# Kernel tuning notes

Hardware: AMD Instinct MI355X
Metric: run time of the kernel (lower is better)

Reference implementation:

```python
import jax, jax.numpy as jnp
import numpy as np

N_NODES = 15000
N_EDGES = 300000
N_RADIAL = 8
N_SPEC = 16
ZMAX = 64
CUTOFF = 5.0
LMAX = 2
NCHANNELS = 128


def bessel_basis(r, dim, rc):
    # b_n(r) = sqrt(2/rc) * sin(n*pi*r/rc) / r , n = 1..dim
    n = jnp.arange(1, dim + 1, dtype=r.dtype)
    return jnp.sqrt(2.0 / rc) * jnp.sin(n[None, :] * (jnp.pi / rc) * r[:, None]) / r[:, None]


def spherical_harmonics_l2(u):
    # Real solid harmonics of unit vectors up to l=2 (Racah/L2-style constants), 9 components
    x, y, z = u[:, 0], u[:, 1], u[:, 2]
    s3 = 3.0 ** 0.5
    s5 = 5.0 ** 0.5
    s15 = 15.0 ** 0.5
    one = jnp.ones_like(x)
    return jnp.stack([
        one,
        s3 * x, s3 * y, s3 * z,
        s15 * x * y, s15 * y * z,
        0.5 * s5 * (3.0 * z * z - 1.0),
        s15 * x * z, 0.5 * s15 * (x * x - y * y),
    ], axis=-1)  # [E, 9]


def setup_inputs() -> dict:
    key = jax.random.key(0)
    ks = jax.random.split(key, 8)
    vec = jax.random.normal(ks[0], (N_EDGES, 3), dtype=jnp.float32)
    distances = jnp.linalg.norm(vec, axis=-1) + 1e-3  # positive, consistent with vec
    switch = jax.random.uniform(ks[1], (N_EDGES,), dtype=jnp.float32)
    species_table = jax.random.normal(ks[2], (ZMAX, N_SPEC), dtype=jnp.float32)
    nbasis = N_RADIAL * N_SPEC
    W0 = jax.random.normal(ks[3], (nbasis, 2 * NCHANNELS), dtype=jnp.float32) / jnp.sqrt(nbasis)
    W1 = jax.random.normal(ks[4], (nbasis, 2 * NCHANNELS), dtype=jnp.float32) / jnp.sqrt(nbasis)
    W2 = jax.random.normal(ks[5], (nbasis, 2 * NCHANNELS), dtype=jnp.float32) / jnp.sqrt(nbasis)
    species = jax.random.randint(ks[6], (N_NODES,), 0, ZMAX)
    edge_src = jnp.sort(jax.random.randint(ks[7], (N_EDGES,), 0, N_NODES))
    edge_dst = jax.random.randint(jax.random.fold_in(key, 7), (N_EDGES,), 0, N_NODES)
    return {
        "distances": distances, "vec": vec, "switch": switch,
        "species_table": species_table, "W0": W0, "W1": W1, "W2": W2,
        "species": species, "edge_src": edge_src, "edge_dst": edge_dst,
    }


def reference(distances, vec, switch, species_table, W0, W1, W2, species, edge_src, edge_dst):
    n_nodes = species.shape[0]
    # radial basis * switch: [E, nr]
    rb = bessel_basis(distances, N_RADIAL, CUTOFF) * switch[:, None]
    senc = species_table[species]  # [N, ns]
    # edge-wise outer product radial x species -> [E, nr*ns]
    Dij = (rb[:, :, None] * senc[edge_dst, None, :]).reshape(rb.shape[0], -1)
    Y = spherical_harmonics_l2(vec / distances[:, None])  # [E, 9]
    # outer product with SH then scatter-sum to nodes: [N, 9, nbasis]
    rhoi = jax.ops.segment_sum(Dij[:, None, :] * Y[:, :, None], edge_src, num_segments=n_nodes)
    xis = [senc, rhoi[:, 0, :]]
    for l, W in enumerate((W0, W1, W2)):
        rhoil = rhoi[:, l * l:(l + 1) * (l + 1), :]  # [N, 2l+1, nbasis]
        xy = jnp.einsum('nmb,bc->nmc', rhoil, W)      # [N, 2l+1, 2*nchannels]
        xl, yl = jnp.split(xy, 2, axis=-1)
        xis.append((xl * yl).sum(axis=1) / (2 * l + 1) ** 0.5)
    return jnp.concatenate(xis, axis=-1)  # [N, ns + nbasis + 3*nchannels]
```

## Files before the change

### kernel.cpp

```cpp
#include <hip/hip_runtime.h>
#include <math.h>

#define N_NODES 15000
#define NPAD    15008
#define N_EDGES 300000
#define NCH     128
#define OUT_COLS 528
#define ES      300032
#define NCHUNK  (ES / 32)
#define YROWS   17
#define CHB     (YROWS * 32)

typedef _Float16 half8   __attribute__((ext_vector_type(8)));
typedef short    short8  __attribute__((ext_vector_type(8)));
typedef float    floatx4 __attribute__((ext_vector_type(4)));

#define WF_BYTES    (3 * 256 * 128 * 2)
#define RP_OFF      WF_BYTES
#define RP_BYTES    61440
#define SPE_OFF     (RP_OFF + RP_BYTES)
#define SPE_BYTES   ((size_t)ES * 2)
#define YF_OFF      (SPE_OFF + SPE_BYTES)
#define YF_BYTES    ((size_t)NCHUNK * CHB * 2 + 256)

#define PREP_EDGE_BLOCKS 1172
#define PREP_WF_BLOCKS   384
#define PREP_RP_BLOCKS   59
#define PREP_BLOCKS (PREP_EDGE_BLOCKS + PREP_WF_BLOCKS + PREP_RP_BLOCKS)

__device__ __forceinline__ size_t wf_pos(int l, int c, int k) {
    int h = c >> 7, cc = c & 127;
    int ct = cc >> 4, nI = cc & 15;
    int K = k >> 5, q = (k >> 3) & 3, j = k & 7;
    return ((size_t)((((l * 8 + ct) * 2 + h) * 4 + K) * 64 + q * 16 + nI)) * 8 + j;
}

__global__ __launch_bounds__(256) void prep_kernel(
    const float* __restrict__ dist, const float* __restrict__ vec,
    const float* __restrict__ sw,   const int* __restrict__ species,
    const int* __restrict__ edst,   const int* __restrict__ esrc,
    const float* __restrict__ W0, const float* __restrict__ W1,
    const float* __restrict__ W2,
    _Float16* __restrict__ Yf, short* __restrict__ spE,
    _Float16* __restrict__ WF,  int* __restrict__ row_ptr)
{
    const int b = blockIdx.x, tid = threadIdx.x;
    if (b < PREP_EDGE_BLOCKS) {
        int e = b * 256 + tid;
        if (e >= N_EDGES) return;

        const float bnorm = 0.6324555320336759f;
        const float s3  = 1.7320508075688772f;
        const float s5  = 2.2360679774997896f;
        const float s15 = 3.872983346207417f;
        const float cstep = 3.14159265358979323846f / 5.0f;

        float r    = dist[e];
        float invr = 1.0f / r;
        float g    = bnorm * invr * sw[e];
        float x = vec[3*e+0] * invr;
        float y = vec[3*e+1] * invr;
        float z = vec[3*e+2] * invr;

        spE[e] = (short)species[edst[e]];

        _Float16* yb = Yf + (size_t)(e >> 5) * CHB + (e & 31);
        yb[0 * 32] = (_Float16)1.0f;
        yb[1 * 32] = (_Float16)(s3 * x);
        yb[2 * 32] = (_Float16)(s3 * y);
        yb[3 * 32] = (_Float16)(s3 * z);
        yb[4 * 32] = (_Float16)(s15 * x * y);
        yb[5 * 32] = (_Float16)(s15 * y * z);
        yb[6 * 32] = (_Float16)(0.5f * s5 * (3.0f * z * z - 1.0f));
        yb[7 * 32] = (_Float16)(s15 * x * z);
        yb[8 * 32] = (_Float16)(0.5f * s15 * (x * x - y * y));
        #pragma unroll
        for (int n = 0; n < 8; ++n)
            yb[(9 + n) * 32] = (_Float16)(g * __sinf((float)(n + 1) * cstep * r));
    } else if (b < PREP_EDGE_BLOCKS + PREP_WF_BLOCKS) {
        int idx = (b - PREP_EDGE_BLOCKS) * 256 + tid;
        int l = idx >> 15;
        int c = (idx >> 7) & 255;
        int k = idx & 127;
        const float* W = (l == 0) ? W0 : ((l == 1) ? W1 : W2);
        WF[wf_pos(l, c, k)] = (_Float16)W[k * 256 + c];
    } else {
        int i = (b - PREP_EDGE_BLOCKS - PREP_WF_BLOCKS) * 256 + tid;
        if (i > NPAD) return;
        int lo = 0, hi = N_EDGES;
        while (lo < hi) { int mid = (lo + hi) >> 1; if (esrc[mid] < i) lo = mid + 1; else hi = mid; }
        row_ptr[i] = lo;
    }
}

__global__ __launch_bounds__(256) void main_kernel(
    const _Float16* __restrict__ Yf, const short* __restrict__ spE,
    const float* __restrict__ stab,  const int* __restrict__ row_ptr,
    const _Float16* __restrict__ WF, const int* __restrict__ species,
    float* __restrict__ out)
{
    __shared__ _Float16 stabL[64 * 16];
    __shared__ __align__(16) _Float16 srho[144 * 136];

    const int tid  = threadIdx.x;
    const int wave = tid >> 6;
    const int lane = tid & 63;
    const int q    = lane >> 4;
    const int nI   = lane & 15;
    const int node0 = blockIdx.x * 16;

    #pragma unroll
    for (int j = 0; j < 4; ++j) stabL[tid * 4 + j] = (_Float16)stab[tid * 4 + j];
    __syncthreads();

    for (int i = 0; i < 4; ++i) {
        const int n16 = 4 * wave + i;
        const int node = node0 + n16;
        const int lo = row_ptr[node], hi = row_ptr[node + 1];

        floatx4 acc[5];
        #pragma unroll
        for (int t = 0; t < 5; ++t) acc[t] = (floatx4){0.f, 0.f, 0.f, 0.f};

        for (int k0 = (lo & ~31); k0 < hi; k0 += 32) {
            short8 sp8 = *(const short8*)(spE + k0 + q * 8);
            half8 bfr;
            #pragma unroll
            for (int j = 0; j < 8; ++j) {
                int e = k0 + q * 8 + j;
                bool valid = (e >= lo) && (e < hi);
                int spv = valid ? (int)sp8[j] : 0;
                _Float16 v = stabL[spv * 16 + nI];
                bfr[j] = valid ? v : (_Float16)0;
            }
            const _Float16* yb = Yf + (size_t)(k0 >> 5) * CHB + q * 8;
            #pragma unroll
            for (int t = 0; t < 5; ++t) {
                int row = t * 16 + nI;
                int m = row >> 3;
                int n = row & 7;
                half8 Y8 = *(const half8*)(yb + m * 32);
                half8 F8 = *(const half8*)(yb + (9 + n) * 32);
                half8 a = Y8 * F8;
                acc[t] = __builtin_amdgcn_mfma_f32_16x16x32_f16(a, bfr, acc[t], 0, 0, 0);
            }
        }

        #pragma unroll
        for (int t = 0; t < 5; ++t)
            #pragma unroll
            for (int r = 0; r < 4; ++r) {
                int row = t * 16 + q * 4 + r;
                if (row < 72) {
                    int m = row >> 3, nrad = row & 7;
                    int k = nrad * 16 + nI;
                    int K = k >> 5, qq = (k >> 3) & 3, j = k & 7;
                    srho[((m * 4 + K) * 4 + qq) * 136 + n16 * 8 + j] = (_Float16)acc[t][r];
                }
            }
    }
    __syncthreads();

    {
        int nn = tid >> 4, c = tid & 15;
        int node = node0 + nn;
        if (node < N_NODES) {
            float* o = out + (size_t)node * OUT_COLS;
            o[c] = stab[species[node] * 16 + c];
            int c0 = c * 8;
            int K = c0 >> 5, qq = (c0 >> 3) & 3;
            half8 h = *(const half8*)&srho[(K * 4 + qq) * 136 + nn * 8];
            #pragma unroll
            for (int j = 0; j < 8; ++j) o[16 + c0 + j] = (float)h[j];
        }
    }

    const int   mstart[3] = {0, 1, 4};
    const int   mcount[3] = {1, 3, 5};
    const float scl[3] = {1.0f, 0.5773502691896258f, 0.4472135954999579f};

    #pragma unroll
    for (int l = 0; l < 3; ++l) {
        half8 Bf[2][2][4];
        #pragma unroll
        for (int cp = 0; cp < 2; ++cp)
            #pragma unroll
            for (int h = 0; h < 2; ++h) {
                int ct = 2 * wave + cp;
                const _Float16* bp = WF +
                    ((size_t)((((l * 8 + ct) * 2 + h) * 4) * 64 + lane)) * 8;
                #pragma unroll
                for (int K = 0; K < 4; ++K)
                    Bf[cp][h][K] = *(const half8*)(bp + (size_t)K * 512);
            }

        floatx4 P0 = {0.f, 0.f, 0.f, 0.f};
        floatx4 P1 = {0.f, 0.f, 0.f, 0.f};

        #pragma unroll
        for (int mi = 0; mi < mcount[l]; ++mi) {
            int m = mstart[l] + mi;
            half8 Af[4];
            #pragma unroll
            for (int K = 0; K < 4; ++K)
                Af[K] = *(const half8*)&srho[((m * 4 + K) * 4 + q) * 136 + nI * 8];

            #pragma unroll
            for (int cp = 0; cp < 2; ++cp) {
                floatx4 Cx = {0.f, 0.f, 0.f, 0.f};
                floatx4 Cy = {0.f, 0.f, 0.f, 0.f};
                #pragma unroll
                for (int K = 0; K < 4; ++K) {
                    Cx = __builtin_amdgcn_mfma_f32_16x16x32_f16(Af[K], Bf[cp][0][K], Cx, 0, 0, 0);
                    Cy = __builtin_amdgcn_mfma_f32_16x16x32_f16(Af[K], Bf[cp][1][K], Cy, 0, 0, 0);
                }
                if (cp == 0) P0 += Cx * Cy; else P1 += Cx * Cy;
            }
        }

        #pragma unroll
        for (int cp = 0; cp < 2; ++cp) {
            floatx4 P = cp ? P1 : P0;
            int c = 144 + l * NCH + 16 * (2 * wave + cp) + nI;
            #pragma unroll
            for (int r = 0; r < 4; ++r) {
                int node = node0 + q * 4 + r;
                if (node < N_NODES)
                    out[(size_t)node * OUT_COLS + c] = P[r] * scl[l];
            }
        }
    }
}

extern "C" void kernel_launch(void* const* d_in, const int* in_sizes, int n_in,
                              void* d_out, int out_size, void* d_ws, size_t ws_size,
                              hipStream_t stream) {
    const float* distances = (const float*)d_in[0];
    const float* vec       = (const float*)d_in[1];
    const float* sw        = (const float*)d_in[2];
    const float* stab      = (const float*)d_in[3];
    const float* W0        = (const float*)d_in[4];
    const float* W1        = (const float*)d_in[5];
    const float* W2        = (const float*)d_in[6];
    const int*   species   = (const int*)d_in[7];
    const int*   esrc      = (const int*)d_in[8];
    const int*   edst      = (const int*)d_in[9];
    float* out = (float*)d_out;

    _Float16* WF     = (_Float16*)d_ws;
    int*      rowptr = (int*)((char*)d_ws + RP_OFF);
    short*    spE    = (short*)((char*)d_ws + SPE_OFF);
    _Float16* Yf     = (_Float16*)((char*)d_ws + YF_OFF);

    prep_kernel<<<PREP_BLOCKS, 256, 0, stream>>>(
        distances, vec, sw, species, edst, esrc, W0, W1, W2,
        Yf, spE, WF, rowptr);
    main_kernel<<<NPAD / 16, 256, 0, stream>>>(
        Yf, spE, stab, rowptr, WF, species, out);
}
```

Measured before the change: 116.8 us.

## Fuse per-edge feature computation and row-pointer search into main kernel

```diff
diff --git a/kernel.cpp b/kernel.cpp
--- a/kernel.cpp
+++ b/kernel.cpp
@@ -6,27 +6,12 @@
 #define N_EDGES 300000
 #define NCH     128
 #define OUT_COLS 528
-#define ES      300032
-#define NCHUNK  (ES / 32)
-#define YROWS   17
-#define CHB     (YROWS * 32)
+#define TE      256
+#define TCH     (TE / 32)
 
 typedef _Float16 half8   __attribute__((ext_vector_type(8)));
 typedef short    short8  __attribute__((ext_vector_type(8)));
 typedef float    floatx4 __attribute__((ext_vector_type(4)));
-
-#define WF_BYTES    (3 * 256 * 128 * 2)
-#define RP_OFF      WF_BYTES
-#define RP_BYTES    61440
-#define SPE_OFF     (RP_OFF + RP_BYTES)
-#define SPE_BYTES   ((size_t)ES * 2)
-#define YF_OFF      (SPE_OFF + SPE_BYTES)
-#define YF_BYTES    ((size_t)NCHUNK * CHB * 2 + 256)
-
-#define PREP_EDGE_BLOCKS 1172
-#define PREP_WF_BLOCKS   384
-#define PREP_RP_BLOCKS   59
-#define PREP_BLOCKS (PREP_EDGE_BLOCKS + PREP_WF_BLOCKS + PREP_RP_BLOCKS)
 
 __device__ __forceinline__ size_t wf_pos(int l, int c, int k) {
     int h = c >> 7, cc = c & 127;
@@ -36,71 +21,30 @@
 }
 
 __global__ __launch_bounds__(256) void prep_kernel(
+    const float* __restrict__ W0, const float* __restrict__ W1,
+    const float* __restrict__ W2, _Float16* __restrict__ WF)
+{
+    int idx = blockIdx.x * 256 + threadIdx.x;
+    if (idx >= 98304) return;
+    int l = idx >> 15;
+    int c = (idx >> 7) & 255;
+    int k = idx & 127;
+    const float* W = (l == 0) ? W0 : ((l == 1) ? W1 : W2);
+    WF[wf_pos(l, c, k)] = (_Float16)W[k * 256 + c];
+}
+
+__global__ __launch_bounds__(256) void main_kernel(
     const float* __restrict__ dist, const float* __restrict__ vec,
-    const float* __restrict__ sw,   const int* __restrict__ species,
-    const int* __restrict__ edst,   const int* __restrict__ esrc,
-    const float* __restrict__ W0, const float* __restrict__ W1,
-    const float* __restrict__ W2,
-    _Float16* __restrict__ Yf, short* __restrict__ spE,
-    _Float16* __restrict__ WF,  int* __restrict__ row_ptr)
-{
-    const int b = blockIdx.x, tid = threadIdx.x;
-    if (b < PREP_EDGE_BLOCKS) {
-        int e = b * 256 + tid;
-        if (e >= N_EDGES) return;
-
-        const float bnorm = 0.6324555320336759f;
-        const float s3  = 1.7320508075688772f;
-        const float s5  = 2.2360679774997896f;
-        const float s15 = 3.872983346207417f;
-        const float cstep = 3.14159265358979323846f / 5.0f;
-
-        float r    = dist[e];
-        float invr = 1.0f / r;
-        float g    = bnorm * invr * sw[e];
-        float x = vec[3*e+0] * invr;
-        float y = vec[3*e+1] * invr;
-        float z = vec[3*e+2] * invr;
-
-        spE[e] = (short)species[edst[e]];
-
-        _Float16* yb = Yf + (size_t)(e >> 5) * CHB + (e & 31);
-        yb[0 * 32] = (_Float16)1.0f;
-        yb[1 * 32] = (_Float16)(s3 * x);
-        yb[2 * 32] = (_Float16)(s3 * y);
-        yb[3 * 32] = (_Float16)(s3 * z);
-        yb[4 * 32] = (_Float16)(s15 * x * y);
-        yb[5 * 32] = (_Float16)(s15 * y * z);
-        yb[6 * 32] = (_Float16)(0.5f * s5 * (3.0f * z * z - 1.0f));
-        yb[7 * 32] = (_Float16)(s15 * x * z);
-        yb[8 * 32] = (_Float16)(0.5f * s15 * (x * x - y * y));
-        #pragma unroll
-        for (int n = 0; n < 8; ++n)
-            yb[(9 + n) * 32] = (_Float16)(g * __sinf((float)(n + 1) * cstep * r));
-    } else if (b < PREP_EDGE_BLOCKS + PREP_WF_BLOCKS) {
-        int idx = (b - PREP_EDGE_BLOCKS) * 256 + tid;
-        int l = idx >> 15;
-        int c = (idx >> 7) & 255;
-        int k = idx & 127;
-        const float* W = (l == 0) ? W0 : ((l == 1) ? W1 : W2);
-        WF[wf_pos(l, c, k)] = (_Float16)W[k * 256 + c];
-    } else {
-        int i = (b - PREP_EDGE_BLOCKS - PREP_WF_BLOCKS) * 256 + tid;
-        if (i > NPAD) return;
-        int lo = 0, hi = N_EDGES;
-        while (lo < hi) { int mid = (lo + hi) >> 1; if (esrc[mid] < i) lo = mid + 1; else hi = mid; }
-        row_ptr[i] = lo;
-    }
-}
-
-__global__ __launch_bounds__(256) void main_kernel(
-    const _Float16* __restrict__ Yf, const short* __restrict__ spE,
-    const float* __restrict__ stab,  const int* __restrict__ row_ptr,
-    const _Float16* __restrict__ WF, const int* __restrict__ species,
+    const float* __restrict__ sw,   const float* __restrict__ stab,
+    const int* __restrict__ species, const int* __restrict__ esrc,
+    const int* __restrict__ edst,   const _Float16* __restrict__ WF,
     float* __restrict__ out)
 {
     __shared__ _Float16 stabL[64 * 16];
     __shared__ __align__(16) _Float16 srho[144 * 136];
+    __shared__ __align__(16) _Float16 stage[TCH * 17 * 32];
+    __shared__ __align__(16) short spL[TE];
+    __shared__ int rpL[17];
 
     const int tid  = threadIdx.x;
     const int wave = tid >> 6;
@@ -109,43 +53,100 @@
     const int nI   = lane & 15;
     const int node0 = blockIdx.x * 16;
 
+    const float bnorm = 0.6324555320336759f;
+    const float s3  = 1.7320508075688772f;
+    const float s5  = 2.2360679774997896f;
+    const float s15 = 3.872983346207417f;
+    const float cstep = 3.14159265358979323846f / 5.0f;
+
     #pragma unroll
     for (int j = 0; j < 4; ++j) stabL[tid * 4 + j] = (_Float16)stab[tid * 4 + j];
+    if (tid < 17) {
+        int i = node0 + tid;
+        int lo = 0, hi = N_EDGES;
+        while (lo < hi) { int mid = (lo + hi) >> 1; if (esrc[mid] < i) lo = mid + 1; else hi = mid; }
+        rpL[tid] = lo;
+    }
     __syncthreads();
 
+    const int blo = rpL[0] & ~31;
+    const int bhi = rpL[16];
+    int LO[5];
+    #pragma unroll
+    for (int i = 0; i < 5; ++i) LO[i] = rpL[4 * wave + i];
+
+    floatx4 acc[4][5];
+    #pragma unroll
+    for (int i = 0; i < 4; ++i)
+        #pragma unroll
+        for (int t = 0; t < 5; ++t) acc[i][t] = (floatx4){0.f, 0.f, 0.f, 0.f};
+
+    for (int t0 = blo; t0 < bhi; t0 += TE) {
+        __syncthreads();
+        {
+            int e = t0 + tid;
+            float r = 1.0f, gv = 0.0f, x = 0.0f, y = 0.0f, z = 0.0f;
+            int sp = 0;
+            if (e < N_EDGES) {
+                r = dist[e];
+                float invr = 1.0f / r;
+                gv = bnorm * invr * sw[e];
+                x = vec[3*e+0] * invr;
+                y = vec[3*e+1] * invr;
+                z = vec[3*e+2] * invr;
+                sp = species[edst[e]];
+            }
+            spL[tid] = (short)sp;
+            _Float16* sb = &stage[(size_t)(tid >> 5) * (17 * 32) + (tid & 31)];
+            sb[0 * 32] = (_Float16)1.0f;
+            sb[1 * 32] = (_Float16)(s3 * x);
+            sb[2 * 32] = (_Float16)(s3 * y);
+            sb[3 * 32] = (_Float16)(s3 * z);
+            sb[4 * 32] = (_Float16)(s15 * x * y);
+            sb[5 * 32] = (_Float16)(s15 * y * z);
+            sb[6 * 32] = (_Float16)(0.5f * s5 * (3.0f * z * z - 1.0f));
+            sb[7 * 32] = (_Float16)(s15 * x * z);
+            sb[8 * 32] = (_Float16)(0.5f * s15 * (x * x - y * y));
+            #pragma unroll
+            for (int n = 0; n < 8; ++n)
+                sb[(9 + n) * 32] = (_Float16)(gv * __sinf((float)(n + 1) * cstep * r));
+        }
+        __syncthreads();
+
+        #pragma unroll
+        for (int i = 0; i < 4; ++i) {
+            const int lo = LO[i], hi = LO[i + 1];
+            int k0s = lo & ~31; if (k0s < t0) k0s = t0;
+            int k0e = hi;       if (k0e > t0 + TE) k0e = t0 + TE;
+            for (int k0 = k0s; k0 < k0e; k0 += 32) {
+                const int cc = (k0 - t0) >> 5;
+                short8 sp8 = *(const short8*)&spL[cc * 32 + q * 8];
+                half8 bfr;
+                #pragma unroll
+                for (int j = 0; j < 8; ++j) {
+                    int e = k0 + q * 8 + j;
+                    bool valid = (e >= lo) && (e < hi);
+                    _Float16 v = stabL[(int)sp8[j] * 16 + nI];
+                    bfr[j] = valid ? v : (_Float16)0;
+                }
+                const _Float16* yb = &stage[(size_t)cc * (17 * 32) + q * 8];
+                #pragma unroll
+                for (int t = 0; t < 5; ++t) {
+                    int row = t * 16 + nI;
+                    int m = row >> 3;
+                    int n = row & 7;
+                    half8 Y8 = *(const half8*)(yb + m * 32);
+                    half8 F8 = *(const half8*)(yb + (9 + n) * 32);
+                    half8 a = Y8 * F8;
+                    acc[i][t] = __builtin_amdgcn_mfma_f32_16x16x32_f16(a, bfr, acc[i][t], 0, 0, 0);
+                }
+            }
+        }
+    }
+
+    #pragma unroll
     for (int i = 0; i < 4; ++i) {
         const int n16 = 4 * wave + i;
-        const int node = node0 + n16;
-        const int lo = row_ptr[node], hi = row_ptr[node + 1];
-
-        floatx4 acc[5];
-        #pragma unroll
-        for (int t = 0; t < 5; ++t) acc[t] = (floatx4){0.f, 0.f, 0.f, 0.f};
-
-        for (int k0 = (lo & ~31); k0 < hi; k0 += 32) {
-            short8 sp8 = *(const short8*)(spE + k0 + q * 8);
-            half8 bfr;
-            #pragma unroll
-            for (int j = 0; j < 8; ++j) {
-                int e = k0 + q * 8 + j;
-                bool valid = (e >= lo) && (e < hi);
-                int spv = valid ? (int)sp8[j] : 0;
-                _Float16 v = stabL[spv * 16 + nI];
-                bfr[j] = valid ? v : (_Float16)0;
-            }
-            const _Float16* yb = Yf + (size_t)(k0 >> 5) * CHB + q * 8;
-            #pragma unroll
-            for (int t = 0; t < 5; ++t) {
-                int row = t * 16 + nI;
-                int m = row >> 3;
-                int n = row & 7;
-                half8 Y8 = *(const half8*)(yb + m * 32);
-                half8 F8 = *(const half8*)(yb + (9 + n) * 32);
-                half8 a = Y8 * F8;
-                acc[t] = __builtin_amdgcn_mfma_f32_16x16x32_f16(a, bfr, acc[t], 0, 0, 0);
-            }
-        }
-
         #pragma unroll
         for (int t = 0; t < 5; ++t)
             #pragma unroll
@@ -155,7 +156,7 @@
                     int m = row >> 3, nrad = row & 7;
                     int k = nrad * 16 + nI;
                     int K = k >> 5, qq = (k >> 3) & 3, j = k & 7;
-                    srho[((m * 4 + K) * 4 + qq) * 136 + n16 * 8 + j] = (_Float16)acc[t][r];
+                    srho[((m * 4 + K) * 4 + qq) * 136 + n16 * 8 + j] = (_Float16)acc[i][t][r];
                 }
             }
     }
@@ -247,14 +248,9 @@
     const int*   edst      = (const int*)d_in[9];
     float* out = (float*)d_out;
 
-    _Float16* WF     = (_Float16*)d_ws;
-    int*      rowptr = (int*)((char*)d_ws + RP_OFF);
-    short*    spE    = (short*)((char*)d_ws + SPE_OFF);
-    _Float16* Yf     = (_Float16*)((char*)d_ws + YF_OFF);
-
-    prep_kernel<<<PREP_BLOCKS, 256, 0, stream>>>(
-        distances, vec, sw, species, edst, esrc, W0, W1, W2,
-        Yf, spE, WF, rowptr);
+    _Float16* WF = (_Float16*)d_ws;
+
+    prep_kernel<<<384, 256, 0, stream>>>(W0, W1, W2, WF);
     main_kernel<<<NPAD / 16, 256, 0, stream>>>(
-        Yf, spE, stab, rowptr, WF, species, out);
-}
+        distances, vec, sw, stab, species, esrc, edst, WF, out);
+}
```

Result: slower. 121.5 us (+4.1%).
